# Kernel tuning notes

Hardware: AMD Instinct MI355X
Metric: run time of the kernel (lower is better)

## Reference

```python
import jax, jax.numpy as jnp
import numpy as np

B, CIN, CCTX, K, V, T, KS = 8, 512, 512, 64, 256, 1024, 23
EPS = 1e-5


def _bn(z, gamma, beta):
    # train-mode BatchNorm1d over (batch, time) per channel, biased variance
    mean = jnp.mean(z, axis=(0, 2), keepdims=True)
    var = jnp.mean((z - mean) ** 2, axis=(0, 2), keepdims=True)
    return (z - mean) * jax.lax.rsqrt(var + EPS) * gamma[None, :, None] + beta[None, :, None]


def setup_inputs() -> dict:
    key = jax.random.key(0)
    ks = jax.random.split(key, 10)
    x = jax.random.normal(ks[0], (B, CIN, T), dtype=jnp.float32)
    context = jax.random.normal(ks[1], (B, CCTX, T), dtype=jnp.float32)
    Wq = jax.random.normal(ks[2], (K, CIN), dtype=jnp.float32) * (CIN ** -0.5)
    bq = jnp.zeros((K,), dtype=jnp.float32)
    Wk = jax.random.normal(ks[3], (K, CCTX), dtype=jnp.float32) * (CCTX ** -0.5)
    bk = jnp.zeros((K,), dtype=jnp.float32)
    Wv = jax.random.normal(ks[4], (V, CCTX), dtype=jnp.float32) * (CCTX ** -0.5)
    bv = jnp.zeros((V,), dtype=jnp.float32)
    gamma_q = jnp.ones((K,), dtype=jnp.float32)
    beta_q = jnp.zeros((K,), dtype=jnp.float32)
    gamma_v = jnp.ones((V,), dtype=jnp.float32)
    beta_v = jnp.zeros((V,), dtype=jnp.float32)
    pos_w = jax.random.normal(ks[5], (K, KS), dtype=jnp.float32) * (KS ** -0.5)
    pos_b = jnp.zeros((K,), dtype=jnp.float32)
    return {"x": x, "context": context, "Wq": Wq, "bq": bq, "Wk": Wk, "bk": bk,
            "Wv": Wv, "bv": bv, "gamma_q": gamma_q, "beta_q": beta_q,
            "gamma_v": gamma_v, "beta_v": beta_v, "pos_w": pos_w, "pos_b": pos_b}


def reference(x, context, Wq, bq, Wk, bk, Wv, bv,
              gamma_q, beta_q, gamma_v, beta_v, pos_w, pos_b):
    # 1x1 conv1d == channel matmul
    queries = jnp.einsum('bct,kc->bkt', x, Wq) + bq[None, :, None]          # (B,K,T)
    keys = jnp.einsum('bct,kc->bkt', context, Wk) + bk[None, :, None]       # (B,K,T)
    values = jnp.einsum('bct,vc->bvt', context, Wv) + bv[None, :, None]     # (B,V,T)

    norm_keys = jax.nn.softmax(keys, axis=-1)                               # softmax over T
    queries = _bn(queries, gamma_q, beta_q)
    values = _bn(values, gamma_v, beta_v)

    q_t = jnp.transpose(queries, (0, 2, 1))                                 # (B,T,K)
    v_t = jnp.transpose(values, (0, 2, 1))                                  # (B,T,V)

    content_lambda = jnp.einsum('bkt,btv->bkv', norm_keys, v_t)             # (B,K,V)

    # positional conv2d: kernel (K,1,KS,1), padding (KS//2, 0) along T
    lhs = v_t[:, None, :, :]                                                # (B,1,T,V)
    rhs = pos_w[:, None, :, None]                                           # (K,1,KS,1)
    pl = jax.lax.conv_general_dilated(
        lhs, rhs, window_strides=(1, 1),
        padding=[(KS // 2, KS // 2), (0, 0)],
        dimension_numbers=('NCHW', 'OIHW', 'NCHW'))
    pl = pl + pos_b[None, :, None, None]                                    # (B,K,T,V)
    pl = jnp.transpose(pl, (0, 2, 1, 3))                                    # (B,T,K,V)

    content_out = jnp.einsum('btk,bkv->btv', q_t, content_lambda)           # (B,T,V)
    positional_out = jnp.einsum('btk,btkv->btv', q_t, pl)                   # (B,T,V)

    return jnp.transpose(content_out + positional_out, (0, 2, 1))           # (B,V,T)
```

## Files before the change

### kernel.cpp

```cpp
#include <hip/hip_runtime.h>
#include <math.h>

#define B_ 8
#define CIN_ 512
#define K_ 64
#define V_ 256
#define T_ 1024
#define KS_ 23
#define EPS_ 1e-5f
#define NTC_ 16

typedef __attribute__((ext_vector_type(8))) short bf16x8;
typedef __attribute__((ext_vector_type(4))) float f32x4;

__device__ __forceinline__ unsigned short f2bf(float f) {
    union { float f; unsigned u; } x; x.f = f;
    unsigned r = x.u + 0x7fffu + ((x.u >> 16) & 1u);
    return (unsigned short)(r >> 16);
}
__device__ __forceinline__ float bf2f(unsigned short h) {
    union { unsigned u; float f; } x; x.u = ((unsigned)h) << 16;
    return x.f;
}

__global__ __launch_bounds__(256) void prep_kernel(
    const float* __restrict__ x, const float* __restrict__ ctx,
    const float* __restrict__ Wq, const float* __restrict__ Wk,
    const float* __restrict__ Wv,
    unsigned short* __restrict__ xT, unsigned short* __restrict__ cT,
    unsigned short* __restrict__ Wb, float* __restrict__ stat)
{
    __shared__ unsigned short sh[64][72];
    const int tid = threadIdx.x;
    const int id = blockIdx.x;
    if (id < 2048) {
        const int t0 = (id & 15) * 64, c0 = ((id >> 4) & 7) * 64;
        const int z = id >> 7, b = z & 7, which = z >> 3;
        const float* src = which ? ctx : x;
        unsigned short* dst = which ? cT : xT;
        const int cl = tid >> 2, qq = tid & 3;
        const float* row = src + ((size_t)b * CIN_ + c0 + cl) * T_ + t0 + qq * 16;
        #pragma unroll
        for (int u = 0; u < 4; u++) {
            float4 f = *(const float4*)(row + 4 * u);
            sh[qq * 16 + 4 * u + 0][cl] = f2bf(f.x);
            sh[qq * 16 + 4 * u + 1][cl] = f2bf(f.y);
            sh[qq * 16 + 4 * u + 2][cl] = f2bf(f.z);
            sh[qq * 16 + 4 * u + 3][cl] = f2bf(f.w);
        }
        __syncthreads();
        const int tl = tid >> 2;
        unsigned short* orow = dst + ((size_t)b * T_ + t0 + tl) * CIN_ + c0 + qq * 16;
        *(bf16x8*)(orow)     = *(bf16x8*)&sh[tl][qq * 16];
        *(bf16x8*)(orow + 8) = *(bf16x8*)&sh[tl][qq * 16 + 8];
    } else {
        const int wid = id - 2048;
        if (wid == 0 && tid < 160)
            ((float4*)stat)[tid] = make_float4(0.f, 0.f, 0.f, 0.f);
        const int i4 = wid * 256 + tid;
        const int n1 = K_ * CIN_ / 4, n2 = 2 * K_ * CIN_ / 4;
        const float* src; int off;
        if (i4 < n1)      { src = Wq; off = i4; }
        else if (i4 < n2) { src = Wk; off = i4 - n1; }
        else              { src = Wv; off = i4 - n2; }
        float4 f = ((const float4*)src)[off];
        ushort4 h;
        h.x = f2bf(f.x); h.y = f2bf(f.y); h.z = f2bf(f.z); h.w = f2bf(f.w);
        *(ushort4*)(Wb + (size_t)i4 * 4) = h;
    }
}

__global__ __launch_bounds__(256) void proj_mfma3(
    const unsigned short* __restrict__ xT, const unsigned short* __restrict__ cT,
    const unsigned short* __restrict__ Wb,
    const float* __restrict__ bq, const float* __restrict__ bk,
    const float* __restrict__ bv,
    float* __restrict__ k_buf, float* __restrict__ v_raw,
    unsigned short* __restrict__ qT, float* __restrict__ stat)
{
    __shared__ unsigned short Wt[64][72];
    __shared__ unsigned short Xt[128][72];
    const int tid = threadIdx.x;
    const int b = blockIdx.z, t0 = blockIdx.x * 128, yb = blockIdx.y;

    const unsigned short* in; const unsigned short* W; const float* bias;
    float* outp = nullptr; int ch0 = 0; float* ssum = nullptr; float* ssq = nullptr;
    if (yb == 0)      { in = xT; W = Wb;             bias = bq;
                        ssum = stat; ssq = stat + 64; ch0 = 0; }
    else if (yb == 1) { in = cT; W = Wb + K_ * CIN_; bias = bk;
                        outp = k_buf + (size_t)b * K_ * T_; }
    else { int m0 = (yb - 2) * 64; in = cT;
           W = Wb + 2 * K_ * CIN_ + (size_t)m0 * CIN_; bias = bv + m0;
           outp = v_raw + ((size_t)b * V_ + m0) * T_;
           ssum = stat + 128; ssq = stat + 384; ch0 = m0; }

    const int lane = tid & 63, w = tid >> 6;
    const int col = lane & 15, quad = lane >> 4;
    const int wm = tid >> 2, wp = tid & 3;
    const int xt = tid >> 1, xh = tid & 1;

    f32x4 acc[8];
    #pragma unroll
    for (int j = 0; j < 8; j++) acc[j] = (f32x4){0.f, 0.f, 0.f, 0.f};

    for (int c0 = 0; c0 < CIN_; c0 += 64) {
        {
            const unsigned short* ws = W + (size_t)wm * CIN_ + c0 + wp * 16;
            *(bf16x8*)&Wt[wm][wp * 16]     = *(const bf16x8*)(ws);
            *(bf16x8*)&Wt[wm][wp * 16 + 8] = *(const bf16x8*)(ws + 8);
            const unsigned short* xs = in + ((size_t)b * T_ + t0 + xt) * CIN_ + c0 + xh * 32;
            #pragma unroll
            for (int u = 0; u < 4; u++)
                *(bf16x8*)&Xt[xt][xh * 32 + 8 * u] = *(const bf16x8*)(xs + 8 * u);
        }
        __syncthreads();
        #pragma unroll
        for (int ks = 0; ks < 2; ks++) {
            const int kc = ks * 32 + quad * 8;
            bf16x8 af = *(bf16x8*)&Wt[w * 16 + col][kc];
            #pragma unroll
            for (int j = 0; j < 8; j++) {
                bf16x8 bfr = *(bf16x8*)&Xt[j * 16 + col][kc];
                acc[j] = __builtin_amdgcn_mfma_f32_16x16x32_bf16(af, bfr, acc[j], 0, 0, 0);
            }
        }
        __syncthreads();
    }

    float bias_v[4], s[4], sq[4];
    #pragma unroll
    for (int r = 0; r < 4; r++) {
        bias_v[r] = bias[w * 16 + quad * 4 + r];
        s[r] = 0.f; sq[r] = 0.f;
    }
    #pragma unroll
    for (int j = 0; j < 8; j++) {
        float o[4];
        #pragma unroll
        for (int r = 0; r < 4; r++) {
            o[r] = acc[j][r] + bias_v[r];
            s[r] += o[r]; sq[r] += o[r] * o[r];
        }
        if (yb == 0) {
            ushort4 h;
            h.x = f2bf(o[0]); h.y = f2bf(o[1]); h.z = f2bf(o[2]); h.w = f2bf(o[3]);
            *(ushort4*)(qT + ((size_t)b * T_ + t0 + j * 16 + col) * K_ + w * 16 + quad * 4) = h;
        } else {
            #pragma unroll
            for (int r = 0; r < 4; r++)
                outp[(size_t)(w * 16 + quad * 4 + r) * T_ + t0 + j * 16 + col] = o[r];
        }
    }
    if (ssum) {
        #pragma unroll
        for (int r = 0; r < 4; r++) {
            float sv = s[r], qv = sq[r];
            #pragma unroll
            for (int off = 1; off < 16; off <<= 1) {
                sv += __shfl_xor(sv, off, 64);
                qv += __shfl_xor(qv, off, 64);
            }
            if (col == 0) {
                int ch = ch0 + w * 16 + quad * 4 + r;
                atomicAdd(&ssum[ch], sv);
                atomicAdd(&ssq[ch], qv);
            }
        }
    }
}

__global__ __launch_bounds__(256) void softmax_kernel(float* __restrict__ k_buf)
{
    __shared__ float red[256];
    const int tid = threadIdx.x;
    float4* row = (float4*)(k_buf + (size_t)blockIdx.x * T_);
    float4 v = row[tid];
    float mx = fmaxf(fmaxf(v.x, v.y), fmaxf(v.z, v.w));
    red[tid] = mx; __syncthreads();
    for (int st = 128; st > 0; st >>= 1) {
        if (tid < st) red[tid] = fmaxf(red[tid], red[tid + st]);
        __syncthreads();
    }
    mx = red[0]; __syncthreads();
    float4 e;
    e.x = __expf(v.x - mx); e.y = __expf(v.y - mx);
    e.z = __expf(v.z - mx); e.w = __expf(v.w - mx);
    red[tid] = e.x + e.y + e.z + e.w; __syncthreads();
    for (int st = 128; st > 0; st >>= 1) {
        if (tid < st) red[tid] += red[tid + st];
        __syncthreads();
    }
    float inv = 1.f / red[0];
    e.x *= inv; e.y *= inv; e.z *= inv; e.w *= inv;
    row[tid] = e;
}

__global__ __launch_bounds__(256) void lambda_kernel3(
    const float* __restrict__ k_buf, const float* __restrict__ v_raw,
    float* __restrict__ clp)
{
    __shared__ __align__(16) float nks[K_][68];
    __shared__ __align__(16) float vls[64][68];
    const int tid = threadIdx.x;
    const int b = blockIdx.z, v0 = blockIdx.y * 64, tc = blockIdx.x, t0 = tc * 64;
    {
        const int r = tid >> 2, q = tid & 3;
        const float* nrow = k_buf + ((size_t)b * K_ + r) * T_ + t0;
        const float* vrow = v_raw + ((size_t)b * V_ + v0 + r) * T_ + t0;
        #pragma unroll
        for (int i = 0; i < 4; i++) {
            int c4 = q + 4 * i;
            float4 g = *(const float4*)(nrow + 4 * c4);
            *(float4*)&nks[r][4 * c4] = g;
            float4 h = *(const float4*)(vrow + 4 * c4);
            vls[4 * c4 + 0][r] = h.x; vls[4 * c4 + 1][r] = h.y;
            vls[4 * c4 + 2][r] = h.z; vls[4 * c4 + 3][r] = h.w;
        }
    }
    __syncthreads();
    const int tv = tid & 15, tk = tid >> 4;
    float4 acc[4];
    #pragma unroll
    for (int i = 0; i < 4; i++) acc[i] = make_float4(0.f, 0.f, 0.f, 0.f);
    for (int tt = 0; tt < 16; tt++) {
        float4 w0 = *(float4*)&vls[4 * tt + 0][4 * tv];
        float4 w1 = *(float4*)&vls[4 * tt + 1][4 * tv];
        float4 w2 = *(float4*)&vls[4 * tt + 2][4 * tv];
        float4 w3 = *(float4*)&vls[4 * tt + 3][4 * tv];
        #pragma unroll
        for (int i = 0; i < 4; i++) {
            float4 n = *(float4*)&nks[4 * tk + i][4 * tt];
            acc[i] += w0 * n.x + w1 * n.y + w2 * n.z + w3 * n.w;
        }
    }
    #pragma unroll
    for (int i = 0; i < 4; i++)
        *(float4*)&clp[(((size_t)b * NTC_ + tc) * K_ + 4 * tk + i) * V_ + v0 + 4 * tv] = acc[i];
}

__global__ __launch_bounds__(256) void prep_cl_kernel2(
    const float* __restrict__ clp, const float* __restrict__ stat,
    const float* __restrict__ gq, const float* __restrict__ betaq,
    const float* __restrict__ gv, const float* __restrict__ betav,
    unsigned short* __restrict__ clb2, float* __restrict__ hterm)
{
    __shared__ float qsc[64], qsh[64], red[4][64];
    const int tid = threadIdx.x;
    const int b = blockIdx.y, v0 = blockIdx.x * 64;
    const float inv_n = 1.f / (B_ * T_);
    if (tid < 64) {
        float mean = stat[tid] * inv_n;
        float var  = stat[64 + tid] * inv_n - mean * mean;
        float sc = gq[tid] * rsqrtf(var + EPS_);
        qsc[tid] = sc; qsh[tid] = betaq[tid] - mean * sc;
    }
    const int vl = tid & 63, kq = tid >> 6;
    const int c = v0 + vl;
    float vmean = stat[128 + c] * inv_n;
    float vvar  = stat[384 + c] * inv_n - vmean * vmean;
    float vsv = gv[c] * rsqrtf(vvar + EPS_);
    float vhv = betav[c] - vmean * vsv;
    __syncthreads();
    float h = 0.f;
    for (int kk = 0; kk < 16; kk++) {
        int k = kq * 16 + kk;
        float a = 0.f;
        #pragma unroll
        for (int tc = 0; tc < NTC_; tc++)
            a += clp[(((size_t)b * NTC_ + tc) * K_ + k) * V_ + c];
        float clbv = a * vsv + vhv;
        h += qsh[k] * clbv;
        clb2[((size_t)b * V_ + c) * K_ + k] = f2bf(clbv * qsc[k]);
    }
    red[kq][vl] = h;
    __syncthreads();
    if (tid < 64)
        hterm[(size_t)b * V_ + v0 + tid] =
            red[0][tid] + red[1][tid] + red[2][tid] + red[3][tid];
}

__global__ __launch_bounds__(256) void out_kernel4(
    const unsigned short* __restrict__ qT, const unsigned short* __restrict__ clb2,
    const float* __restrict__ hterm, const float* __restrict__ v_raw,
    const float* __restrict__ stat,
    const float* __restrict__ gq, const float* __restrict__ betaq,
    const float* __restrict__ gv, const float* __restrict__ betav,
    const float* __restrict__ pos_w, const float* __restrict__ pos_b,
    float* __restrict__ out)
{
    __shared__ unsigned short qTt[64][72];
    __shared__ unsigned short clv[64][72];
    __shared__ float vs2T[88][68];
    __shared__ float qpt[64][24];
    __shared__ float pws[64][24];
    __shared__ float qsc[64], qsh[64];
    __shared__ float consts[24];
    __shared__ float hvs[64];
    const int tid = threadIdx.x;
    const int b = blockIdx.z, v0 = blockIdx.y * 64, t0 = blockIdx.x * 64;
    const float inv_n = 1.f / (B_ * T_);

    if (tid < 64) {
        float mean = stat[tid] * inv_n;
        float var  = stat[64 + tid] * inv_n - mean * mean;
        float sc = gq[tid] * rsqrtf(var + EPS_);
        qsc[tid] = sc; qsh[tid] = betaq[tid] - mean * sc;
        hvs[tid] = hterm[(size_t)b * V_ + v0 + tid];
    }
    {
        const int rl = tid >> 2, part = tid & 3;
        const unsigned short* qs = qT + ((size_t)b * T_ + t0 + rl) * K_ + part * 16;
        *(bf16x8*)&qTt[rl][part * 16]     = *(const bf16x8*)(qs);
        *(bf16x8*)&qTt[rl][part * 16 + 8] = *(const bf16x8*)(qs + 8);
        const unsigned short* cs = clb2 + ((size_t)b * V_ + v0 + rl) * K_ + part * 16;
        *(bf16x8*)&clv[rl][part * 16]     = *(const bf16x8*)(cs);
        *(bf16x8*)&clv[rl][part * 16 + 8] = *(const bf16x8*)(cs + 8);
    }
    {
        const int vl = tid >> 2, qq = tid & 3;
        const int c = v0 + vl;
        float vmean = stat[128 + c] * inv_n;
        float vvar  = stat[384 + c] * inv_n - vmean * vmean;
        float vsv = gv[c] * rsqrtf(vvar + EPS_);
        float vhv = betav[c] - vmean * vsv;
        const float* vrow = v_raw + ((size_t)b * V_ + c) * T_;
        #pragma unroll
        for (int i = 0; i < 22; i++) {
            int cc = qq + 4 * i;
            if (cc < 86) {
                int t = t0 + cc - 11;
                vs2T[cc][vl] = (t >= 0 && t < T_) ? vrow[t] * vsv + vhv : 0.f;
            }
        }
    }
    __syncthreads();

    for (int idx = tid; idx < K_ * 24; idx += 256) {
        int k = idx / 24, s = idx % 24;
        pws[k][s] = qsc[k] * (s < KS_ ? pos_w[k * KS_ + s] : pos_b[k]);
    }
    if (tid < 24) {
        float cs = 0.f;
        for (int k = 0; k < K_; k++)
            cs += qsh[k] * (tid < KS_ ? pos_w[k * KS_ + tid] : pos_b[k]);
        consts[tid] = cs;
    }
    __syncthreads();

    {
        const int t = tid >> 2, sg = tid & 3, s0 = sg * 6;
        float a[6];
        #pragma unroll
        for (int u = 0; u < 6; u++) a[u] = consts[s0 + u];
        #pragma unroll
        for (int kb = 0; kb < 8; kb++) {
            bf16x8 qv = *(bf16x8*)&qTt[t][kb * 8];
            #pragma unroll
            for (int j = 0; j < 8; j++) {
                float q = bf2f((unsigned short)qv[j]);
                #pragma unroll
                for (int u = 0; u < 6; u++) a[u] += q * pws[kb * 8 + j][s0 + u];
            }
        }
        #pragma unroll
        for (int u = 0; u < 6; u++) qpt[t][s0 + u] = a[u];
    }
    __syncthreads();

    const int lane = tid & 63, w = tid >> 6;
    const int col = lane & 15, quad = lane >> 4;

    f32x4 acc[4];
    #pragma unroll
    for (int tf = 0; tf < 4; tf++) acc[tf] = (f32x4){0.f, 0.f, 0.f, 0.f};

    #pragma unroll
    for (int ks = 0; ks < 2; ks++) {
        const int kc = ks * 32 + quad * 8;
        bf16x8 af = *(bf16x8*)&clv[w * 16 + col][kc];
        #pragma unroll
        for (int tf = 0; tf < 4; tf++) {
            bf16x8 bq = *(bf16x8*)&qTt[tf * 16 + col][kc];
            acc[tf] = __builtin_amdgcn_mfma_f32_16x16x32_bf16(af, bq, acc[tf], 0, 0, 0);
        }
    }

    const int vb = w * 16 + quad * 4;
    float4 hv4 = *(float4*)&hvs[vb];
    #pragma unroll
    for (int tf = 0; tf < 4; tf++) {
        const int lt = tf * 16 + col;
        float qv[24];
        #pragma unroll
        for (int u = 0; u < 6; u++)
            *(float4*)&qv[4 * u] = *(float4*)&qpt[lt][4 * u];
        float4 a; a.x = acc[tf][0]; a.y = acc[tf][1]; a.z = acc[tf][2]; a.w = acc[tf][3];
        #pragma unroll
        for (int s = 0; s < KS_; s++) {
            float4 wv = *(float4*)&vs2T[lt + s][vb];
            a.x += qv[s] * wv.x; a.y += qv[s] * wv.y;
            a.z += qv[s] * wv.z; a.w += qv[s] * wv.w;
        }
        float base = qv[23];
        a.x += base + hv4.x; a.y += base + hv4.y;
        a.z += base + hv4.z; a.w += base + hv4.w;
        float* ap = (float*)&a;
        #pragma unroll
        for (int r = 0; r < 4; r++)
            out[((size_t)b * V_ + v0 + vb + r) * T_ + t0 + lt] = ap[r];
    }
}

extern "C" void kernel_launch(void* const* d_in, const int* in_sizes, int n_in,
                              void* d_out, int out_size, void* d_ws, size_t ws_size,
                              hipStream_t stream)
{
    const float* x     = (const float*)d_in[0];
    const float* ctx   = (const float*)d_in[1];
    const float* Wq    = (const float*)d_in[2];
    const float* bq    = (const float*)d_in[3];
    const float* Wk    = (const float*)d_in[4];
    const float* bk    = (const float*)d_in[5];
    const float* Wv    = (const float*)d_in[6];
    const float* bv    = (const float*)d_in[7];
    const float* gq    = (const float*)d_in[8];
    const float* betaq = (const float*)d_in[9];
    const float* gv    = (const float*)d_in[10];
    const float* betav = (const float*)d_in[11];
    const float* pos_w = (const float*)d_in[12];
    const float* pos_b = (const float*)d_in[13];
    float* out = (float*)d_out;

    float* ws    = (float*)d_ws;
    float* k_buf = ws;
    float* v_raw = k_buf + (size_t)B_ * K_ * T_;
    float* clp   = v_raw + (size_t)B_ * V_ * T_;
    float* stat  = clp + (size_t)B_ * NTC_ * K_ * V_;
    float* hterm = stat + 640;
    unsigned short* xT   = (unsigned short*)(hterm + (size_t)B_ * V_);
    unsigned short* cT   = xT + (size_t)B_ * T_ * CIN_;
    unsigned short* Wb   = cT + (size_t)B_ * T_ * CIN_;
    unsigned short* qT   = Wb + (size_t)(2 * K_ + V_) * CIN_;
    unsigned short* clb2 = qT + (size_t)B_ * T_ * K_;

    prep_kernel<<<dim3(2048 + 192), 256, 0, stream>>>(
        x, ctx, Wq, Wk, Wv, xT, cT, Wb, stat);
    proj_mfma3<<<dim3(T_ / 128, 6, B_), 256, 0, stream>>>(
        xT, cT, Wb, bq, bk, bv, k_buf, v_raw, qT, stat);
    softmax_kernel<<<dim3(B_ * K_), 256, 0, stream>>>(k_buf);
    lambda_kernel3<<<dim3(NTC_, V_ / 64, B_), 256, 0, stream>>>(k_buf, v_raw, clp);
    prep_cl_kernel2<<<dim3(V_ / 64, B_), 256, 0, stream>>>(
        clp, stat, gq, betaq, gv, betav, clb2, hterm);
    out_kernel4<<<dim3(T_ / 64, V_ / 64, B_), 256, 0, stream>>>(
        qT, clb2, hterm, v_raw, stat, gq, betaq, gv, betav, pos_w, pos_b, out);
}
```

Measured before the change: 160.4 us.

## Fuse key softmax into projection and lambda kernels via online max/sum partials

Removes the standalone softmax kernel. The projection kernel now computes per-128-column online max and exp-sum partials for the key rows and writes them to a small buffer. The lambda kernel merges the eight partials per row and applies exp and normalisation while loading keys into shared memory. This saves one launch and a full read-write pass over the key buffer, at the cost of redundant exp work, since each lambda block recomputes exps for its tile across the four V blocks.

```diff
diff --git a/kernel.cpp b/kernel.cpp
--- a/kernel.cpp
+++ b/kernel.cpp
@@ -70,13 +70,14 @@
     }
 }
 
-__global__ __launch_bounds__(256) void proj_mfma3(
+__global__ __launch_bounds__(256) void proj_mfma4(
     const unsigned short* __restrict__ xT, const unsigned short* __restrict__ cT,
     const unsigned short* __restrict__ Wb,
     const float* __restrict__ bq, const float* __restrict__ bk,
     const float* __restrict__ bv,
     float* __restrict__ k_buf, float* __restrict__ v_raw,
-    unsigned short* __restrict__ qT, float* __restrict__ stat)
+    unsigned short* __restrict__ qT, float* __restrict__ stat,
+    float* __restrict__ kml)
 {
     __shared__ unsigned short Wt[64][72];
     __shared__ unsigned short Xt[128][72];
@@ -127,11 +128,11 @@
         __syncthreads();
     }
 
-    float bias_v[4], s[4], sq[4];
+    float bias_v[4], s[4], sq[4], mr[4], lr[4];
     #pragma unroll
     for (int r = 0; r < 4; r++) {
         bias_v[r] = bias[w * 16 + quad * 4 + r];
-        s[r] = 0.f; sq[r] = 0.f;
+        s[r] = 0.f; sq[r] = 0.f; mr[r] = -1e30f; lr[r] = 0.f;
     }
     #pragma unroll
     for (int j = 0; j < 8; j++) {
@@ -149,9 +150,35 @@
             #pragma unroll
             for (int r = 0; r < 4; r++)
                 outp[(size_t)(w * 16 + quad * 4 + r) * T_ + t0 + j * 16 + col] = o[r];
-        }
-    }
-    if (ssum) {
+            if (yb == 1) {
+                #pragma unroll
+                for (int r = 0; r < 4; r++) {
+                    float mn = fmaxf(mr[r], o[r]);
+                    lr[r] = lr[r] * __expf(mr[r] - mn) + __expf(o[r] - mn);
+                    mr[r] = mn;
+                }
+            }
+        }
+    }
+    if (yb == 1) {
+        #pragma unroll
+        for (int r = 0; r < 4; r++) {
+            float m = mr[r], l = lr[r];
+            #pragma unroll
+            for (int off = 1; off < 16; off <<= 1) {
+                float mo = __shfl_xor(m, off, 64);
+                float lo = __shfl_xor(l, off, 64);
+                float mn = fmaxf(m, mo);
+                l = l * __expf(m - mn) + lo * __expf(mo - mn);
+                m = mn;
+            }
+            if (col == 0) {
+                int row = w * 16 + quad * 4 + r;
+                float* p = kml + (((size_t)b * K_ + row) * 8 + (t0 >> 7)) * 2;
+                p[0] = m; p[1] = l;
+            }
+        }
+    } else {
         #pragma unroll
         for (int r = 0; r < 4; r++) {
             float sv = s[r], qv = sq[r];
@@ -169,48 +196,40 @@
     }
 }
 
-__global__ __launch_bounds__(256) void softmax_kernel(float* __restrict__ k_buf)
-{
-    __shared__ float red[256];
-    const int tid = threadIdx.x;
-    float4* row = (float4*)(k_buf + (size_t)blockIdx.x * T_);
-    float4 v = row[tid];
-    float mx = fmaxf(fmaxf(v.x, v.y), fmaxf(v.z, v.w));
-    red[tid] = mx; __syncthreads();
-    for (int st = 128; st > 0; st >>= 1) {
-        if (tid < st) red[tid] = fmaxf(red[tid], red[tid + st]);
-        __syncthreads();
-    }
-    mx = red[0]; __syncthreads();
-    float4 e;
-    e.x = __expf(v.x - mx); e.y = __expf(v.y - mx);
-    e.z = __expf(v.z - mx); e.w = __expf(v.w - mx);
-    red[tid] = e.x + e.y + e.z + e.w; __syncthreads();
-    for (int st = 128; st > 0; st >>= 1) {
-        if (tid < st) red[tid] += red[tid + st];
-        __syncthreads();
-    }
-    float inv = 1.f / red[0];
-    e.x *= inv; e.y *= inv; e.z *= inv; e.w *= inv;
-    row[tid] = e;
-}
-
-__global__ __launch_bounds__(256) void lambda_kernel3(
+__global__ __launch_bounds__(256) void lambda_kernel4(
     const float* __restrict__ k_buf, const float* __restrict__ v_raw,
-    float* __restrict__ clp)
+    const float* __restrict__ kml, float* __restrict__ clp)
 {
     __shared__ __align__(16) float nks[K_][68];
     __shared__ __align__(16) float vls[64][68];
+    __shared__ float mrow[64], lrow[64];
     const int tid = threadIdx.x;
     const int b = blockIdx.z, v0 = blockIdx.y * 64, tc = blockIdx.x, t0 = tc * 64;
+
+    if (tid < 64) {
+        const float2* p = (const float2*)(kml + ((size_t)b * K_ + tid) * 16);
+        float m = -1e30f, l = 0.f;
+        #pragma unroll
+        for (int sgi = 0; sgi < 8; sgi++) {
+            float2 ml = p[sgi];
+            float mn = fmaxf(m, ml.x);
+            l = l * __expf(m - mn) + ml.y * __expf(ml.x - mn);
+            m = mn;
+        }
+        mrow[tid] = m; lrow[tid] = 1.f / l;
+    }
+    __syncthreads();
     {
         const int r = tid >> 2, q = tid & 3;
         const float* nrow = k_buf + ((size_t)b * K_ + r) * T_ + t0;
         const float* vrow = v_raw + ((size_t)b * V_ + v0 + r) * T_ + t0;
+        const float mr = mrow[r], li = lrow[r];
         #pragma unroll
         for (int i = 0; i < 4; i++) {
             int c4 = q + 4 * i;
             float4 g = *(const float4*)(nrow + 4 * c4);
+            g.x = __expf(g.x - mr) * li; g.y = __expf(g.y - mr) * li;
+            g.z = __expf(g.z - mr) * li; g.w = __expf(g.w - mr) * li;
             *(float4*)&nks[r][4 * c4] = g;
             float4 h = *(const float4*)(vrow + 4 * c4);
             vls[4 * c4 + 0][r] = h.x; vls[4 * c4 + 1][r] = h.y;
@@ -437,7 +456,8 @@
     float* clp   = v_raw + (size_t)B_ * V_ * T_;
     float* stat  = clp + (size_t)B_ * NTC_ * K_ * V_;
     float* hterm = stat + 640;
-    unsigned short* xT   = (unsigned short*)(hterm + (size_t)B_ * V_);
+    float* kml   = hterm + (size_t)B_ * V_;
+    unsigned short* xT   = (unsigned short*)(kml + (size_t)B_ * K_ * 16);
     unsigned short* cT   = xT + (size_t)B_ * T_ * CIN_;
     unsigned short* Wb   = cT + (size_t)B_ * T_ * CIN_;
     unsigned short* qT   = Wb + (size_t)(2 * K_ + V_) * CIN_;
@@ -445,10 +465,9 @@
 
     prep_kernel<<<dim3(2048 + 192), 256, 0, stream>>>(
         x, ctx, Wq, Wk, Wv, xT, cT, Wb, stat);
-    proj_mfma3<<<dim3(T_ / 128, 6, B_), 256, 0, stream>>>(
-        xT, cT, Wb, bq, bk, bv, k_buf, v_raw, qT, stat);
-    softmax_kernel<<<dim3(B_ * K_), 256, 0, stream>>>(k_buf);
-    lambda_kernel3<<<dim3(NTC_, V_ / 64, B_), 256, 0, stream>>>(k_buf, v_raw, clp);
+    proj_mfma4<<<dim3(T_ / 128, 6, B_), 256, 0, stream>>>(
+        xT, cT, Wb, bq, bk, bv, k_buf, v_raw, qT, stat, kml);
+    lambda_kernel4<<<dim3(NTC_, V_ / 64, B_), 256, 0, stream>>>(k_buf, v_raw, kml, clp);
     prep_cl_kernel2<<<dim3(V_ / 64, B_), 256, 0, stream>>>(
         clp, stat, gq, betaq, gv, betav, clb2, hterm);
     out_kernel4<<<dim3(T_ / 64, V_ / 64, B_), 256, 0, stream>>>(
```

New measurement: 155.6 us. 1.03x faster.
